# Kernel optimization log

Hardware: AMD Instinct MI355X
Metric: run time of the kernel (lower is better)

## Reference

```python
import jax, jax.numpy as jnp
import numpy as np

B, T, D, H = 4096, 100, 64, 128
N_RK4 = 4  # fixed RK4 substeps per observation gap (deterministic stand-in for adaptive odeint)


def setup_inputs() -> dict:
    key = jax.random.key(0)
    ks = jax.random.split(key, 12)
    x_seq = jax.random.normal(ks[0], (B, T, D), dtype=jnp.float32)
    # strictly increasing shared timestamps (source only uses t_seq[0, :])
    t0 = jnp.cumsum(jax.random.uniform(ks[1], (T,), dtype=jnp.float32) * 0.1 + 0.01)
    t_seq = jnp.broadcast_to(t0, (B, T))
    s_h = 1.0 / np.sqrt(H)
    s_d = 1.0 / np.sqrt(D)
    # ODE func: f(h) = tanh(h W1^T + b1) W2^T + b2
    W1 = jax.random.normal(ks[2], (H, H), jnp.float32) * s_h
    b1 = jnp.zeros((H,), jnp.float32)
    W2 = jax.random.normal(ks[3], (H, H), jnp.float32) * s_h * 0.1
    b2 = jnp.zeros((H,), jnp.float32)
    # GRUCell params (PyTorch layout: [3H, in])
    W_ih = jax.random.normal(ks[4], (3 * H, D), jnp.float32) * s_d
    W_hh = jax.random.normal(ks[5], (3 * H, H), jnp.float32) * s_h
    b_ih = jax.random.normal(ks[6], (3 * H,), jnp.float32) * s_h
    b_hh = jax.random.normal(ks[7], (3 * H,), jnp.float32) * s_h
    W_mu = jax.random.normal(ks[8], (H, H), jnp.float32) * s_h
    b_mu = jnp.zeros((H,), jnp.float32)
    W_lv = jax.random.normal(ks[9], (H, H), jnp.float32) * s_h
    b_lv = jnp.zeros((H,), jnp.float32)
    return dict(x_seq=x_seq, t_seq=t_seq, W1=W1, b1=b1, W2=W2, b2=b2,
                W_ih=W_ih, W_hh=W_hh, b_ih=b_ih, b_hh=b_hh,
                W_mu=W_mu, b_mu=b_mu, W_lv=W_lv, b_lv=b_lv)


def _odernn(x_seq, t_seq, W1, b1, W2, b2, W_ih, W_hh, b_ih, b_hh, W_mu, b_mu, W_lv, b_lv):
    Hdim = W1.shape[0]

    def f(h):  # ode_func, autonomous
        return jnp.tanh(h @ W1.T + b1) @ W2.T + b2

    def rk4_jump(h, dt):  # integrate dh/dt = f(h) over dt with N_RK4 substeps
        sub = dt / N_RK4  # scalar
        for _ in range(N_RK4):
            k1 = f(h)
            k2 = f(h + 0.5 * sub * k1)
            k3 = f(h + 0.5 * sub * k2)
            k4 = f(h + sub * k3)
            h = h + (sub / 6.0) * (k1 + 2.0 * k2 + 2.0 * k3 + k4)
        return h

    def gru(x, h):
        gi = x @ W_ih.T + b_ih  # [B, 3H]
        gh = h @ W_hh.T + b_hh
        i_r, i_z, i_n = jnp.split(gi, 3, axis=-1)
        h_r, h_z, h_n = jnp.split(gh, 3, axis=-1)
        r = jax.nn.sigmoid(i_r + h_r)
        z = jax.nn.sigmoid(i_z + h_z)
        n = jnp.tanh(i_n + r * h_n)
        return (1.0 - z) * n + z * h

    t0 = t_seq[0]  # [T] shared times, as in source (t_seq[0, i])
    dt = jnp.concatenate([jnp.zeros((1,), t0.dtype), t0[1:] - t0[:-1]])  # dt[0]=0 -> no jump at i=0
    h0 = jnp.zeros((x_seq.shape[0], Hdim), x_seq.dtype)

    def step(h, inp):
        x_i, dt_i = inp
        h = rk4_jump(h, dt_i)
        h = gru(x_i, h)
        return h, None

    h, _ = jax.lax.scan(step, h0, (jnp.swapaxes(x_seq, 0, 1), dt))
    mu = h @ W_mu.T + b_mu
    logvar = h @ W_lv.T + b_lv
    return mu, logvar


def reference(x_seq, t_seq, W1, b1, W2, b2, W_ih, W_hh, b_ih, b_hh, W_mu, b_mu, W_lv, b_lv):
    return _odernn(x_seq, t_seq, W1, b1, W2, b2, W_ih, W_hh, b_ih, b_hh, W_mu, b_mu, W_lv, b_lv)
```

## Files before the change

kernel.cpp:

```cpp
#include <hip/hip_runtime.h>

#define Bn 4096
#define Tn 100
#define Dn 64
#define Hn 128

typedef _Float16 half8v __attribute__((ext_vector_type(8)));
typedef _Float16 half4v __attribute__((ext_vector_type(4)));
typedef float    float4v __attribute__((ext_vector_type(4)));
typedef float    float2v __attribute__((ext_vector_type(2)));

__device__ __forceinline__ float fast_tanh(float x) {
    float e = __expf(x + x);
    return 1.0f - 2.0f * __builtin_amdgcn_rcpf(e + 1.0f);
}
__device__ __forceinline__ float fast_sig(float x) {
    return __builtin_amdgcn_rcpf(1.0f + __expf(-x));
}
__device__ __forceinline__ float4v tanh4(float4v u) {
    float4v a;
#pragma unroll
    for (int r = 0; r < 4; r++) a[r] = fast_tanh(u[r]);
    return a;
}
__device__ __forceinline__ half4v pack4(float4v v) {
    half4v p;
#pragma unroll
    for (int r = 0; r < 4; r++) p[r] = (_Float16)v[r];
    return p;
}

__device__ __forceinline__ half8v load_wfrag(const float* __restrict__ W, int ld, int n, int k) {
    const float* p = W + (size_t)n * ld + k;
    float4v a = *(const float4v*)p;
    float4v b = *(const float4v*)(p + 4);
    half8v r;
    r[0] = (_Float16)a[0]; r[1] = (_Float16)a[1]; r[2] = (_Float16)a[2]; r[3] = (_Float16)a[3];
    r[4] = (_Float16)b[0]; r[5] = (_Float16)b[1]; r[6] = (_Float16)b[2]; r[7] = (_Float16)b[3];
    return r;
}

__global__ __launch_bounds__(512) void odernn_kernel(
    const float* __restrict__ x_seq, const float* __restrict__ t_seq,
    const float* __restrict__ W1,   const float* __restrict__ b1,
    const float* __restrict__ W2,   const float* __restrict__ b2,
    const float* __restrict__ W_ih, const float* __restrict__ W_hh,
    const float* __restrict__ b_ih, const float* __restrict__ b_hh,
    const float* __restrict__ W_mu, const float* __restrict__ b_mu,
    const float* __restrict__ W_lv, const float* __restrict__ b_lv,
    float* __restrict__ out)
{
    __shared__ _Float16 vbuf[16 * 136];
    __shared__ _Float16 abuf[2][16 * 136];
    __shared__ _Float16 xbuf[16 * 72];
    __shared__ float    ts_l[Tn];
    __shared__ float    c1s[Hn];

    const int tid  = threadIdx.x;
    const int lane = tid & 63;
    const int w    = tid >> 6;
    const int q    = lane >> 4;
    const int m    = lane & 15;
    const int blk  = blockIdx.x;

    if (tid < Tn) ts_l[tid] = t_seq[tid];
    for (int i = tid; i < 16 * 136; i += 512) vbuf[i] = (_Float16)0.f;
    if (tid < Hn) {
        float acc = 0.f;
        const float* r1 = W1 + (size_t)tid * Hn;
#pragma unroll 4
        for (int j = 0; j < Hn; j++) acc += b2[j] * r1[j];
        c1s[tid] = acc;
    }

    const int n0 = 16 * w + m;
    half8v w1f[4], w2f[4], whhf[3][4], wihf[3][2];
#pragma unroll
    for (int kt = 0; kt < 4; kt++) {
        w1f[kt] = load_wfrag(W1, Hn, n0, 32 * kt + q * 8);
        w2f[kt] = load_wfrag(W2, Hn, n0, 32 * kt + q * 8);
    }
#pragma unroll
    for (int g = 0; g < 3; g++) {
        int n = 128 * g + n0;
#pragma unroll
        for (int kt = 0; kt < 4; kt++) whhf[g][kt] = load_wfrag(W_hh, Hn, n, 32 * kt + q * 8);
#pragma unroll
        for (int kt = 0; kt < 2; kt++) wihf[g][kt] = load_wfrag(W_ih, Dn, n, 32 * kt + q * 8);
    }
    float4v b1q = *(const float4v*)(b1 + 16 * w + q * 4);
    float4v b2q = *(const float4v*)(b2 + 16 * w + q * 4);
    float4v bihq[3], bhhq[3];
#pragma unroll
    for (int g = 0; g < 3; g++) {
        bihq[g] = *(const float4v*)(b_ih + 128 * g + 16 * w + q * 4);
        bhhq[g] = *(const float4v*)(b_hh + 128 * g + 16 * w + q * 4);
    }

    float4v accM[4][2];
#pragma unroll
    for (int kt = 0; kt < 4; kt++) {
        float4v zz = {0.f, 0.f, 0.f, 0.f};
        accM[kt][0] = zz; accM[kt][1] = zz;
    }
    {
        const float* w1row = W1 + (size_t)n0 * Hn;
        for (int j = 0; j < Hn; j++) {
            float w1v = w1row[j];
            const float* w2r = W2 + (size_t)j * Hn + q * 8;
#pragma unroll
            for (int kt = 0; kt < 4; kt++) {
                float4v aa = *(const float4v*)(w2r + 32 * kt);
                float4v bb = *(const float4v*)(w2r + 32 * kt + 4);
#pragma unroll
                for (int r = 0; r < 4; r++) {
                    accM[kt][0][r] += w1v * aa[r];
                    accM[kt][1][r] += w1v * bb[r];
                }
            }
        }
    }
    half8v w21f[4];
#pragma unroll
    for (int kt = 0; kt < 4; kt++) {
#pragma unroll
        for (int r = 0; r < 4; r++) {
            w21f[kt][r]     = (_Float16)accM[kt][0][r];
            w21f[kt][r + 4] = (_Float16)accM[kt][1][r];
        }
    }

    float4v h = {0.f, 0.f, 0.f, 0.f};

    const int xrow = tid >> 5;
    const int xcol = (tid & 31) * 2;
    const float* xptr = x_seq + (size_t)(blk * 16 + xrow) * (Tn * Dn) + xcol;
    float2v xreg = *(const float2v*)xptr;

    const int wslot = m * 136 + 16 * w + q * 4;

    auto gemm4 = [&](const half8v* Wf, const _Float16* base, float4v cin) -> float4v {
        const _Float16* p = base + m * 136 + q * 8;
        half8v bf0 = *(const half8v*)(p);
        half8v bf1 = *(const half8v*)(p + 32);
        half8v bf2 = *(const half8v*)(p + 64);
        half8v bf3 = *(const half8v*)(p + 96);
        float4v o1 = cin;
        float4v o2 = {0.f, 0.f, 0.f, 0.f};
        o1 = __builtin_amdgcn_mfma_f32_16x16x32_f16(Wf[0], bf0, o1, 0, 0, 0);
        o2 = __builtin_amdgcn_mfma_f32_16x16x32_f16(Wf[2], bf2, o2, 0, 0, 0);
        o1 = __builtin_amdgcn_mfma_f32_16x16x32_f16(Wf[1], bf1, o1, 0, 0, 0);
        o2 = __builtin_amdgcn_mfma_f32_16x16x32_f16(Wf[3], bf3, o2, 0, 0, 0);
#pragma unroll
        for (int r = 0; r < 4; r++) o1[r] += o2[r];
        return o1;
    };

    float4v c1q;
    __syncthreads();
#pragma unroll
    for (int r = 0; r < 4; r++) c1q[r] = c1s[16 * w + q * 4 + r];
    const float4v zero4 = {0.f, 0.f, 0.f, 0.f};

#pragma unroll 1
    for (int t = 0; t < Tn; ++t) {
        {
            _Float16* xp = xbuf + xrow * 72 + xcol;
            xp[0] = (_Float16)xreg[0]; xp[1] = (_Float16)xreg[1];
        }
        float tc  = ts_l[t];
        float tp  = (t > 0) ? ts_l[t - 1] : tc;
        float sub = (tc - tp) * 0.25f;
        float hs  = 0.5f * sub;
        float s6  = sub * (1.0f / 6.0f);
        __syncthreads();
        if (t + 1 < Tn) xreg = *(const float2v*)(xptr + (t + 1) * Dn);

        float4v gi[3];
        {
            const _Float16* xp = xbuf + m * 72 + q * 8;
            half8v xf0 = *(const half8v*)(xp);
            half8v xf1 = *(const half8v*)(xp + 32);
#pragma unroll
            for (int g = 0; g < 3; g++) {
                float4v acc = bihq[g];
                acc = __builtin_amdgcn_mfma_f32_16x16x32_f16(wihf[g][0], xf0, acc, 0, 0, 0);
                acc = __builtin_amdgcn_mfma_f32_16x16x32_f16(wihf[g][1], xf1, acc, 0, 0, 0);
                gi[g] = acc;
            }
        }
        float4v u_h = gemm4(w1f, vbuf, b1q);

        if (sub != 0.0f) {
            float4v Abar = zero4;
#pragma unroll 1
            for (int s = 0; s < 4; s++) {
                float4v a1 = tanh4(u_h);
                float4v A  = a1;
                *(half4v*)(abuf[0] + wslot) = pack4(a1);
                __syncthreads();
                float4v g = gemm4(w21f, abuf[0], c1q);
                float4v u;
#pragma unroll
                for (int r = 0; r < 4; r++) u[r] = u_h[r] + hs * g[r];
                float4v a2 = tanh4(u);
#pragma unroll
                for (int r = 0; r < 4; r++) A[r] += 2.0f * a2[r];
                *(half4v*)(abuf[1] + wslot) = pack4(a2);
                __syncthreads();
                g = gemm4(w21f, abuf[1], c1q);
#pragma unroll
                for (int r = 0; r < 4; r++) u[r] = u_h[r] + hs * g[r];
                float4v a3 = tanh4(u);
#pragma unroll
                for (int r = 0; r < 4; r++) A[r] += 2.0f * a3[r];
                *(half4v*)(abuf[0] + wslot) = pack4(a3);
                __syncthreads();
                g = gemm4(w21f, abuf[0], c1q);
#pragma unroll
                for (int r = 0; r < 4; r++) u[r] = u_h[r] + sub * g[r];
                float4v a4 = tanh4(u);
#pragma unroll
                for (int r = 0; r < 4; r++) A[r] += a4[r];
                *(half4v*)(abuf[1] + wslot) = pack4(A);
                __syncthreads();
                g = gemm4(w21f, abuf[1], zero4);
#pragma unroll
                for (int r = 0; r < 4; r++) {
                    u_h[r]  += s6 * g[r] + sub * c1q[r];
                    Abar[r] += A[r];
                }
            }
            *(half4v*)(abuf[0] + wslot) = pack4(Abar);
            __syncthreads();
            float4v gw = gemm4(w2f, abuf[0], zero4);
            float fourSub = 4.0f * sub;
#pragma unroll
            for (int r = 0; r < 4; r++) h[r] += s6 * gw[r] + fourSub * b2q[r];
            *(half4v*)(vbuf + wslot) = pack4(h);
            __syncthreads();
        }

        float4v gh[3];
        {
            const _Float16* p = vbuf + m * 136 + q * 8;
            half8v bf0 = *(const half8v*)(p);
            half8v bf1 = *(const half8v*)(p + 32);
            half8v bf2 = *(const half8v*)(p + 64);
            half8v bf3 = *(const half8v*)(p + 96);
#pragma unroll
            for (int g = 0; g < 3; g++) {
                float4v acc = bhhq[g];
                acc = __builtin_amdgcn_mfma_f32_16x16x32_f16(whhf[g][0], bf0, acc, 0, 0, 0);
                acc = __builtin_amdgcn_mfma_f32_16x16x32_f16(whhf[g][1], bf1, acc, 0, 0, 0);
                acc = __builtin_amdgcn_mfma_f32_16x16x32_f16(whhf[g][2], bf2, acc, 0, 0, 0);
                acc = __builtin_amdgcn_mfma_f32_16x16x32_f16(whhf[g][3], bf3, acc, 0, 0, 0);
                gh[g] = acc;
            }
        }
        __syncthreads();

        {
            half4v pk;
#pragma unroll
            for (int r = 0; r < 4; r++) {
                float rr = fast_sig(gi[0][r] + gh[0][r]);
                float zz = fast_sig(gi[1][r] + gh[1][r]);
                float nn = fast_tanh(gi[2][r] + rr * gh[2][r]);
                float hv = (1.0f - zz) * nn + zz * h[r];
                h[r] = hv;
                pk[r] = (_Float16)hv;
            }
            *(half4v*)(vbuf + wslot) = pk;
        }
    }

    __syncthreads();

#pragma unroll
    for (int mat = 0; mat < 2; mat++) {
        const float* Wm = mat ? W_lv : W_mu;
        const float* bm = mat ? b_lv : b_mu;
        float4v acc = *(const float4v*)(bm + 16 * w + q * 4);
        const _Float16* p = vbuf + m * 136 + q * 8;
#pragma unroll
        for (int kt = 0; kt < 4; kt++) {
            half8v af = load_wfrag(Wm, Hn, n0, 32 * kt + q * 8);
            acc = __builtin_amdgcn_mfma_f32_16x16x32_f16(af, *(const half8v*)(p + kt * 32), acc, 0, 0, 0);
        }
        *(float4v*)(out + (size_t)mat * Bn * Hn + (size_t)(blk * 16 + m) * Hn + 16 * w + q * 4) = acc;
    }
}

extern "C" void kernel_launch(void* const* d_in, const int* in_sizes, int n_in,
                              void* d_out, int out_size, void* d_ws, size_t ws_size,
                              hipStream_t stream) {
    (void)in_sizes; (void)n_in; (void)d_ws; (void)ws_size; (void)out_size;
    odernn_kernel<<<dim3(Bn / 16), dim3(512), 0, stream>>>(
        (const float*)d_in[0],  (const float*)d_in[1],  (const float*)d_in[2],
        (const float*)d_in[3],  (const float*)d_in[4],  (const float*)d_in[5],
        (const float*)d_in[6],  (const float*)d_in[7],  (const float*)d_in[8],
        (const float*)d_in[9],  (const float*)d_in[10], (const float*)d_in[11],
        (const float*)d_in[12], (const float*)d_in[13], (float*)d_out);
}
```

Measured before the change: 811.2 us.

## Fold W_hh into ODE jump, use FP8 MFMA for inner ODE GEMMs

Precomputes W_hh·W2 and W_hh·b2 so the GRU hidden-gate projection is computed from the pre-jump state plus a correction from the averaged tanh activations. This removes the separate h write and barrier after the RK4 jump and lets the W1 and W_hh GEMMs on the old state run together. The RK4 inner GEMMs and the correction GEMMs switch from fp16 to fp8 MFMA with a fixed scale of 64 and a permuted shared-memory layout. Launch bounds now request two blocks per CU. The risk is accuracy loss from fp8 weights and activations, plus register pressure from the extra fragments.

```diff
diff --git a/kernel.cpp b/kernel.cpp
--- a/kernel.cpp
+++ b/kernel.cpp
@@ -9,6 +9,7 @@
 typedef _Float16 half4v __attribute__((ext_vector_type(4)));
 typedef float    float4v __attribute__((ext_vector_type(4)));
 typedef float    float2v __attribute__((ext_vector_type(2)));
+typedef long     long2v  __attribute__((ext_vector_type(2)));
 
 __device__ __forceinline__ float fast_tanh(float x) {
     float e = __expf(x + x);
@@ -28,6 +29,16 @@
 #pragma unroll
     for (int r = 0; r < 4; r++) p[r] = (_Float16)v[r];
     return p;
+}
+__device__ __forceinline__ int pack_fp8x4(float a, float b, float c, float d) {
+    int v = __builtin_amdgcn_cvt_pk_fp8_f32(a, b, 0, false);
+    v = __builtin_amdgcn_cvt_pk_fp8_f32(c, d, v, true);
+    return v;
+}
+__device__ __forceinline__ long pack_fp8x8s(float4v a, float4v b, float s) {
+    int lo = pack_fp8x4(a[0]*s, a[1]*s, a[2]*s, a[3]*s);
+    int hi = pack_fp8x4(b[0]*s, b[1]*s, b[2]*s, b[3]*s);
+    return (long)(((unsigned long long)(unsigned)hi << 32) | (unsigned)lo);
 }
 
 __device__ __forceinline__ half8v load_wfrag(const float* __restrict__ W, int ld, int n, int k) {
@@ -40,7 +51,7 @@
     return r;
 }
 
-__global__ __launch_bounds__(512) void odernn_kernel(
+__global__ __launch_bounds__(512, 2) void odernn_kernel(
     const float* __restrict__ x_seq, const float* __restrict__ t_seq,
     const float* __restrict__ W1,   const float* __restrict__ b1,
     const float* __restrict__ W2,   const float* __restrict__ b2,
@@ -51,10 +62,11 @@
     float* __restrict__ out)
 {
     __shared__ _Float16 vbuf[16 * 136];
-    __shared__ _Float16 abuf[2][16 * 136];
+    __shared__ __attribute__((aligned(16))) unsigned char abuf8[2][16 * 144];
     __shared__ _Float16 xbuf[16 * 72];
     __shared__ float    ts_l[Tn];
     __shared__ float    c1s[Hn];
+    __shared__ float    c2s[3 * Hn];
 
     const int tid  = threadIdx.x;
     const int lane = tid & 63;
@@ -71,15 +83,19 @@
 #pragma unroll 4
         for (int j = 0; j < Hn; j++) acc += b2[j] * r1[j];
         c1s[tid] = acc;
+    } else {
+        int i = tid - Hn;
+        float acc = 0.f;
+        const float* rh = W_hh + (size_t)i * Hn;
+#pragma unroll 4
+        for (int j = 0; j < Hn; j++) acc += rh[j] * b2[j];
+        c2s[i] = acc;
     }
 
     const int n0 = 16 * w + m;
-    half8v w1f[4], w2f[4], whhf[3][4], wihf[3][2];
-#pragma unroll
-    for (int kt = 0; kt < 4; kt++) {
-        w1f[kt] = load_wfrag(W1, Hn, n0, 32 * kt + q * 8);
-        w2f[kt] = load_wfrag(W2, Hn, n0, 32 * kt + q * 8);
-    }
+    half8v w1f[4], whhf[3][4], wihf[3][2];
+#pragma unroll
+    for (int kt = 0; kt < 4; kt++) w1f[kt] = load_wfrag(W1, Hn, n0, 32 * kt + q * 8);
 #pragma unroll
     for (int g = 0; g < 3; g++) {
         int n = 128 * g + n0;
@@ -97,37 +113,41 @@
         bhhq[g] = *(const float4v*)(b_hh + 128 * g + 16 * w + q * 4);
     }
 
-    float4v accM[4][2];
+    float4v aM[4][2], aG[3][4][2];
 #pragma unroll
     for (int kt = 0; kt < 4; kt++) {
         float4v zz = {0.f, 0.f, 0.f, 0.f};
-        accM[kt][0] = zz; accM[kt][1] = zz;
+        aM[kt][0] = zz; aM[kt][1] = zz;
+#pragma unroll
+        for (int g = 0; g < 3; g++) { aG[g][kt][0] = zz; aG[g][kt][1] = zz; }
     }
     {
-        const float* w1row = W1 + (size_t)n0 * Hn;
+        const float* w1row = W1   + (size_t)n0 * Hn;
+        const float* h0row = W_hh + (size_t)n0 * Hn;
+        const float* h1row = W_hh + (size_t)(128 + n0) * Hn;
+        const float* h2row = W_hh + (size_t)(256 + n0) * Hn;
         for (int j = 0; j < Hn; j++) {
-            float w1v = w1row[j];
+            float s0 = w1row[j], s1 = h0row[j], s2 = h1row[j], s3 = h2row[j];
             const float* w2r = W2 + (size_t)j * Hn + q * 8;
 #pragma unroll
             for (int kt = 0; kt < 4; kt++) {
                 float4v aa = *(const float4v*)(w2r + 32 * kt);
                 float4v bb = *(const float4v*)(w2r + 32 * kt + 4);
-#pragma unroll
-                for (int r = 0; r < 4; r++) {
-                    accM[kt][0][r] += w1v * aa[r];
-                    accM[kt][1][r] += w1v * bb[r];
-                }
-            }
-        }
-    }
-    half8v w21f[4];
+                aM[kt][0] += s0 * aa;      aM[kt][1] += s0 * bb;
+                aG[0][kt][0] += s1 * aa;   aG[0][kt][1] += s1 * bb;
+                aG[1][kt][0] += s2 * aa;   aG[1][kt][1] += s2 * bb;
+                aG[2][kt][0] += s3 * aa;   aG[2][kt][1] += s3 * bb;
+            }
+        }
+    }
+    long w21f8[4], m2f8[3][4], w2f8[4];
 #pragma unroll
     for (int kt = 0; kt < 4; kt++) {
-#pragma unroll
-        for (int r = 0; r < 4; r++) {
-            w21f[kt][r]     = (_Float16)accM[kt][0][r];
-            w21f[kt][r + 4] = (_Float16)accM[kt][1][r];
-        }
+        w21f8[kt] = pack_fp8x8s(aM[kt][0], aM[kt][1], 64.0f);
+#pragma unroll
+        for (int g = 0; g < 3; g++) m2f8[g][kt] = pack_fp8x8s(aG[g][kt][0], aG[g][kt][1], 64.0f);
+        const float* p = W2 + (size_t)n0 * Hn + 32 * kt + q * 8;
+        w2f8[kt] = pack_fp8x8s(*(const float4v*)p, *(const float4v*)(p + 4), 64.0f);
     }
 
     float4v h = {0.f, 0.f, 0.f, 0.f};
@@ -138,29 +158,33 @@
     float2v xreg = *(const float2v*)xptr;
 
     const int wslot = m * 136 + 16 * w + q * 4;
-
-    auto gemm4 = [&](const half8v* Wf, const _Float16* base, float4v cin) -> float4v {
-        const _Float16* p = base + m * 136 + q * 8;
-        half8v bf0 = *(const half8v*)(p);
-        half8v bf1 = *(const half8v*)(p + 32);
-        half8v bf2 = *(const half8v*)(p + 64);
-        half8v bf3 = *(const half8v*)(p + 96);
-        float4v o1 = cin;
-        float4v o2 = {0.f, 0.f, 0.f, 0.f};
-        o1 = __builtin_amdgcn_mfma_f32_16x16x32_f16(Wf[0], bf0, o1, 0, 0, 0);
-        o2 = __builtin_amdgcn_mfma_f32_16x16x32_f16(Wf[2], bf2, o2, 0, 0, 0);
-        o1 = __builtin_amdgcn_mfma_f32_16x16x32_f16(Wf[1], bf1, o1, 0, 0, 0);
-        o2 = __builtin_amdgcn_mfma_f32_16x16x32_f16(Wf[3], bf3, o2, 0, 0, 0);
-#pragma unroll
-        for (int r = 0; r < 4; r++) o1[r] += o2[r];
-        return o1;
+    const int ppos = 64 * (w >> 2) + 16 * ((2 * (w & 3) + (q >> 1)) & 3)
+                   + 8 * ((w >> 1) & 1) + 4 * (q & 1);
+    const float4v zero4 = {0.f, 0.f, 0.f, 0.f};
+
+    auto store_a = [&](int pp, float4v v) {
+        *(int*)(abuf8[pp] + m * 144 + ppos) = pack_fp8x4(v[0], v[1], v[2], v[3]);
     };
-
-    float4v c1q;
+    auto gemm8 = [&](const long* Wf, int pp) -> float4v {
+        const unsigned char* p = abuf8[pp] + m * 144;
+        long2v L0 = *(const long2v*)(p + q * 16);
+        long2v L1 = *(const long2v*)(p + 64 + q * 16);
+        float4v o1 = zero4, o2 = zero4;
+        o1 = __builtin_amdgcn_mfma_f32_16x16x32_fp8_fp8(Wf[0], L0[0], o1, 0, 0, 0);
+        o2 = __builtin_amdgcn_mfma_f32_16x16x32_fp8_fp8(Wf[2], L1[0], o2, 0, 0, 0);
+        o1 = __builtin_amdgcn_mfma_f32_16x16x32_fp8_fp8(Wf[1], L0[1], o1, 0, 0, 0);
+        o2 = __builtin_amdgcn_mfma_f32_16x16x32_fp8_fp8(Wf[3], L1[1], o2, 0, 0, 0);
+        return o1 + o2;
+    };
+
+    float4v c1q, c2q[3];
     __syncthreads();
 #pragma unroll
     for (int r = 0; r < 4; r++) c1q[r] = c1s[16 * w + q * 4 + r];
-    const float4v zero4 = {0.f, 0.f, 0.f, 0.f};
+#pragma unroll
+    for (int g = 0; g < 3; g++)
+#pragma unroll
+        for (int r = 0; r < 4; r++) c2q[g][r] = c2s[128 * g + 16 * w + q * 4 + r];
 
 #pragma unroll 1
     for (int t = 0; t < Tn; ++t) {
@@ -168,15 +192,18 @@
             _Float16* xp = xbuf + xrow * 72 + xcol;
             xp[0] = (_Float16)xreg[0]; xp[1] = (_Float16)xreg[1];
         }
-        float tc  = ts_l[t];
-        float tp  = (t > 0) ? ts_l[t - 1] : tc;
-        float sub = (tc - tp) * 0.25f;
-        float hs  = 0.5f * sub;
-        float s6  = sub * (1.0f / 6.0f);
+        float tc   = ts_l[t];
+        float tp   = (t > 0) ? ts_l[t - 1] : tc;
+        float sub  = (tc - tp) * 0.25f;
+        float hs   = 0.5f * sub;
+        float s6   = sub * (1.0f / 6.0f);
+        float hs64 = hs * (1.0f / 64.0f);
+        float sb64 = sub * (1.0f / 64.0f);
+        float s664 = s6 * (1.0f / 64.0f);
         __syncthreads();
         if (t + 1 < Tn) xreg = *(const float2v*)(xptr + (t + 1) * Dn);
 
-        float4v gi[3];
+        float4v gi[3], gh[3], u_h;
         {
             const _Float16* xp = xbuf + m * 72 + q * 8;
             half8v xf0 = *(const half8v*)(xp);
@@ -188,66 +215,17 @@
                 acc = __builtin_amdgcn_mfma_f32_16x16x32_f16(wihf[g][1], xf1, acc, 0, 0, 0);
                 gi[g] = acc;
             }
-        }
-        float4v u_h = gemm4(w1f, vbuf, b1q);
-
-        if (sub != 0.0f) {
-            float4v Abar = zero4;
-#pragma unroll 1
-            for (int s = 0; s < 4; s++) {
-                float4v a1 = tanh4(u_h);
-                float4v A  = a1;
-                *(half4v*)(abuf[0] + wslot) = pack4(a1);
-                __syncthreads();
-                float4v g = gemm4(w21f, abuf[0], c1q);
-                float4v u;
-#pragma unroll
-                for (int r = 0; r < 4; r++) u[r] = u_h[r] + hs * g[r];
-                float4v a2 = tanh4(u);
-#pragma unroll
-                for (int r = 0; r < 4; r++) A[r] += 2.0f * a2[r];
-                *(half4v*)(abuf[1] + wslot) = pack4(a2);
-                __syncthreads();
-                g = gemm4(w21f, abuf[1], c1q);
-#pragma unroll
-                for (int r = 0; r < 4; r++) u[r] = u_h[r] + hs * g[r];
-                float4v a3 = tanh4(u);
-#pragma unroll
-                for (int r = 0; r < 4; r++) A[r] += 2.0f * a3[r];
-                *(half4v*)(abuf[0] + wslot) = pack4(a3);
-                __syncthreads();
-                g = gemm4(w21f, abuf[0], c1q);
-#pragma unroll
-                for (int r = 0; r < 4; r++) u[r] = u_h[r] + sub * g[r];
-                float4v a4 = tanh4(u);
-#pragma unroll
-                for (int r = 0; r < 4; r++) A[r] += a4[r];
-                *(half4v*)(abuf[1] + wslot) = pack4(A);
-                __syncthreads();
-                g = gemm4(w21f, abuf[1], zero4);
-#pragma unroll
-                for (int r = 0; r < 4; r++) {
-                    u_h[r]  += s6 * g[r] + sub * c1q[r];
-                    Abar[r] += A[r];
-                }
-            }
-            *(half4v*)(abuf[0] + wslot) = pack4(Abar);
-            __syncthreads();
-            float4v gw = gemm4(w2f, abuf[0], zero4);
-            float fourSub = 4.0f * sub;
-#pragma unroll
-            for (int r = 0; r < 4; r++) h[r] += s6 * gw[r] + fourSub * b2q[r];
-            *(half4v*)(vbuf + wslot) = pack4(h);
-            __syncthreads();
-        }
-
-        float4v gh[3];
-        {
-            const _Float16* p = vbuf + m * 136 + q * 8;
-            half8v bf0 = *(const half8v*)(p);
-            half8v bf1 = *(const half8v*)(p + 32);
-            half8v bf2 = *(const half8v*)(p + 64);
-            half8v bf3 = *(const half8v*)(p + 96);
+            const _Float16* vp = vbuf + m * 136 + q * 8;
+            half8v bf0 = *(const half8v*)(vp);
+            half8v bf1 = *(const half8v*)(vp + 32);
+            half8v bf2 = *(const half8v*)(vp + 64);
+            half8v bf3 = *(const half8v*)(vp + 96);
+            float4v o1 = b1q, o2 = zero4;
+            o1 = __builtin_amdgcn_mfma_f32_16x16x32_f16(w1f[0], bf0, o1, 0, 0, 0);
+            o2 = __builtin_amdgcn_mfma_f32_16x16x32_f16(w1f[2], bf2, o2, 0, 0, 0);
+            o1 = __builtin_amdgcn_mfma_f32_16x16x32_f16(w1f[1], bf1, o1, 0, 0, 0);
+            o2 = __builtin_amdgcn_mfma_f32_16x16x32_f16(w1f[3], bf3, o2, 0, 0, 0);
+            u_h = o1 + o2;
 #pragma unroll
             for (int g = 0; g < 3; g++) {
                 float4v acc = bhhq[g];
@@ -258,7 +236,62 @@
                 gh[g] = acc;
             }
         }
-        __syncthreads();
+
+        if (sub != 0.0f) {
+            float4v Abar = zero4;
+#pragma unroll 1
+            for (int s = 0; s < 4; s++) {
+                float4v a1 = tanh4(u_h);
+                float4v A = a1;
+                store_a(0, a1);
+                __syncthreads();
+                float4v g = gemm8(w21f8, 0);
+                float4v u = u_h + hs64 * g + hs * c1q;
+                float4v a2 = tanh4(u);
+                A += 2.0f * a2;
+                store_a(1, a2);
+                __syncthreads();
+                g = gemm8(w21f8, 1);
+                u = u_h + hs64 * g + hs * c1q;
+                float4v a3 = tanh4(u);
+                A += 2.0f * a3;
+                store_a(0, a3);
+                __syncthreads();
+                g = gemm8(w21f8, 0);
+                u = u_h + sb64 * g + sub * c1q;
+                float4v a4 = tanh4(u);
+                A += a4;
+                store_a(1, A);
+                __syncthreads();
+                g = gemm8(w21f8, 1);
+                u_h += s664 * g + sub * c1q;
+                Abar += A;
+            }
+            store_a(0, Abar);
+            __syncthreads();
+            {
+                const unsigned char* p = abuf8[0] + m * 144;
+                long2v L0 = *(const long2v*)(p + q * 16);
+                long2v L1 = *(const long2v*)(p + 64 + q * 16);
+                float4v o1 = zero4, o2 = zero4;
+                o1 = __builtin_amdgcn_mfma_f32_16x16x32_fp8_fp8(w2f8[0], L0[0], o1, 0, 0, 0);
+                o2 = __builtin_amdgcn_mfma_f32_16x16x32_fp8_fp8(w2f8[2], L1[0], o2, 0, 0, 0);
+                o1 = __builtin_amdgcn_mfma_f32_16x16x32_fp8_fp8(w2f8[1], L0[1], o1, 0, 0, 0);
+                o2 = __builtin_amdgcn_mfma_f32_16x16x32_fp8_fp8(w2f8[3], L1[1], o2, 0, 0, 0);
+                float4v hd = o1 + o2;
+                float fs = 4.0f * sub;
+                h += s664 * hd + fs * b2q;
+#pragma unroll
+                for (int g = 0; g < 3; g++) {
+                    float4v p1 = zero4, p2 = zero4;
+                    p1 = __builtin_amdgcn_mfma_f32_16x16x32_fp8_fp8(m2f8[g][0], L0[0], p1, 0, 0, 0);
+                    p2 = __builtin_amdgcn_mfma_f32_16x16x32_fp8_fp8(m2f8[g][2], L1[0], p2, 0, 0, 0);
+                    p1 = __builtin_amdgcn_mfma_f32_16x16x32_fp8_fp8(m2f8[g][1], L0[1], p1, 0, 0, 0);
+                    p2 = __builtin_amdgcn_mfma_f32_16x16x32_fp8_fp8(m2f8[g][3], L1[1], p2, 0, 0, 0);
+                    gh[g] += s664 * (p1 + p2) + fs * c2q[g];
+                }
+            }
+        }
 
         {
             half4v pk;
```

Measured after the change: 1.048 ms. +29.2%, slower.

## Skip final RK4 state update, move W_ih fragments to LDS, force two waves per EU

Applied to the files above, without the earlier changes.

The last RK4 substep's u_h update (one GEMM and one barrier) is skipped because its result is never used. Only Abar feeds the W2 projection of h. The W_ih weight fragments move from registers to shared memory and are reloaded each timestep, which frees VGPRs. A waves_per_eu(2,2) attribute is added so the compiler targets two waves per EU. The trade is extra LDS reads per step and a possible register-allocation change.

```diff
diff --git a/kernel.cpp b/kernel.cpp
--- a/kernel.cpp
+++ b/kernel.cpp
@@ -5,8 +5,8 @@
 #define Dn 64
 #define Hn 128
 
-typedef _Float16 half8v __attribute__((ext_vector_type(8)));
-typedef _Float16 half4v __attribute__((ext_vector_type(4)));
+typedef _Float16 half8v  __attribute__((ext_vector_type(8)));
+typedef _Float16 half4v  __attribute__((ext_vector_type(4)));
 typedef float    float4v __attribute__((ext_vector_type(4)));
 typedef float    float2v __attribute__((ext_vector_type(2)));
 
@@ -40,7 +40,8 @@
     return r;
 }
 
-__global__ __launch_bounds__(512) void odernn_kernel(
+__global__ __attribute__((amdgpu_flat_work_group_size(512, 512), amdgpu_waves_per_eu(2, 2)))
+void odernn_kernel(
     const float* __restrict__ x_seq, const float* __restrict__ t_seq,
     const float* __restrict__ W1,   const float* __restrict__ b1,
     const float* __restrict__ W2,   const float* __restrict__ b2,
@@ -50,10 +51,11 @@
     const float* __restrict__ W_lv, const float* __restrict__ b_lv,
     float* __restrict__ out)
 {
+    __shared__ float    ts_l[Tn];
     __shared__ _Float16 vbuf[16 * 136];
     __shared__ _Float16 abuf[2][16 * 136];
     __shared__ _Float16 xbuf[16 * 72];
-    __shared__ float    ts_l[Tn];
+    __shared__ _Float16 wih_l[8 * 6 * 64 * 8];
     __shared__ float    c1s[Hn];
 
     const int tid  = threadIdx.x;
@@ -72,22 +74,26 @@
         for (int j = 0; j < Hn; j++) acc += b2[j] * r1[j];
         c1s[tid] = acc;
     }
+#pragma unroll
+    for (int f = 0; f < 6; f++) {
+        int g = f >> 1, kt = f & 1;
+        half8v fr = load_wfrag(W_ih, Dn, 128 * g + 16 * w + m, 32 * kt + q * 8);
+        *(half8v*)(wih_l + ((w * 6 + f) * 64 + lane) * 8) = fr;
+    }
 
     const int n0 = 16 * w + m;
-    half8v w1f[4], w2f[4], whhf[3][4], wihf[3][2];
+    half8v w1f[4], w2f[4], whhf[3][4];
 #pragma unroll
     for (int kt = 0; kt < 4; kt++) {
         w1f[kt] = load_wfrag(W1, Hn, n0, 32 * kt + q * 8);
         w2f[kt] = load_wfrag(W2, Hn, n0, 32 * kt + q * 8);
     }
 #pragma unroll
-    for (int g = 0; g < 3; g++) {
-        int n = 128 * g + n0;
-#pragma unroll
-        for (int kt = 0; kt < 4; kt++) whhf[g][kt] = load_wfrag(W_hh, Hn, n, 32 * kt + q * 8);
-#pragma unroll
-        for (int kt = 0; kt < 2; kt++) wihf[g][kt] = load_wfrag(W_ih, Dn, n, 32 * kt + q * 8);
-    }
+    for (int g = 0; g < 3; g++)
+#pragma unroll
+        for (int kt = 0; kt < 4; kt++)
+            whhf[g][kt] = load_wfrag(W_hh, Hn, 128 * g + n0, 32 * kt + q * 8);
+
     float4v b1q = *(const float4v*)(b1 + 16 * w + q * 4);
     float4v b2q = *(const float4v*)(b2 + 16 * w + q * 4);
     float4v bihq[3], bhhq[3];
@@ -97,11 +103,11 @@
         bhhq[g] = *(const float4v*)(b_hh + 128 * g + 16 * w + q * 4);
     }
 
-    float4v accM[4][2];
+    float4v aM[4][2];
 #pragma unroll
     for (int kt = 0; kt < 4; kt++) {
         float4v zz = {0.f, 0.f, 0.f, 0.f};
-        accM[kt][0] = zz; accM[kt][1] = zz;
+        aM[kt][0] = zz; aM[kt][1] = zz;
     }
     {
         const float* w1row = W1 + (size_t)n0 * Hn;
@@ -110,13 +116,8 @@
             const float* w2r = W2 + (size_t)j * Hn + q * 8;
 #pragma unroll
             for (int kt = 0; kt < 4; kt++) {
-                float4v aa = *(const float4v*)(w2r + 32 * kt);
-                float4v bb = *(const float4v*)(w2r + 32 * kt + 4);
-#pragma unroll
-                for (int r = 0; r < 4; r++) {
-                    accM[kt][0][r] += w1v * aa[r];
-                    accM[kt][1][r] += w1v * bb[r];
-                }
+                aM[kt][0] += w1v * *(const float4v*)(w2r + 32 * kt);
+                aM[kt][1] += w1v * *(const float4v*)(w2r + 32 * kt + 4);
             }
         }
     }
@@ -125,12 +126,13 @@
     for (int kt = 0; kt < 4; kt++) {
 #pragma unroll
         for (int r = 0; r < 4; r++) {
-            w21f[kt][r]     = (_Float16)accM[kt][0][r];
-            w21f[kt][r + 4] = (_Float16)accM[kt][1][r];
+            w21f[kt][r]     = (_Float16)aM[kt][0][r];
+            w21f[kt][r + 4] = (_Float16)aM[kt][1][r];
         }
     }
 
     float4v h = {0.f, 0.f, 0.f, 0.f};
+    const float4v zero4 = {0.f, 0.f, 0.f, 0.f};
 
     const int xrow = tid >> 5;
     const int xcol = (tid & 31) * 2;
@@ -146,21 +148,18 @@
         half8v bf2 = *(const half8v*)(p + 64);
         half8v bf3 = *(const half8v*)(p + 96);
         float4v o1 = cin;
-        float4v o2 = {0.f, 0.f, 0.f, 0.f};
+        float4v o2 = zero4;
         o1 = __builtin_amdgcn_mfma_f32_16x16x32_f16(Wf[0], bf0, o1, 0, 0, 0);
         o2 = __builtin_amdgcn_mfma_f32_16x16x32_f16(Wf[2], bf2, o2, 0, 0, 0);
         o1 = __builtin_amdgcn_mfma_f32_16x16x32_f16(Wf[1], bf1, o1, 0, 0, 0);
         o2 = __builtin_amdgcn_mfma_f32_16x16x32_f16(Wf[3], bf3, o2, 0, 0, 0);
-#pragma unroll
-        for (int r = 0; r < 4; r++) o1[r] += o2[r];
-        return o1;
+        return o1 + o2;
     };
 
     float4v c1q;
     __syncthreads();
 #pragma unroll
     for (int r = 0; r < 4; r++) c1q[r] = c1s[16 * w + q * 4 + r];
-    const float4v zero4 = {0.f, 0.f, 0.f, 0.f};
 
 #pragma unroll 1
     for (int t = 0; t < Tn; ++t) {
@@ -184,8 +183,10 @@
 #pragma unroll
             for (int g = 0; g < 3; g++) {
                 float4v acc = bihq[g];
-                acc = __builtin_amdgcn_mfma_f32_16x16x32_f16(wihf[g][0], xf0, acc, 0, 0, 0);
-                acc = __builtin_amdgcn_mfma_f32_16x16x32_f16(wihf[g][1], xf1, acc, 0, 0, 0);
+                half8v wf0 = *(const half8v*)(wih_l + ((w * 6 + g * 2 + 0) * 64 + lane) * 8);
+                half8v wf1 = *(const half8v*)(wih_l + ((w * 6 + g * 2 + 1) * 64 + lane) * 8);
+                acc = __builtin_amdgcn_mfma_f32_16x16x32_f16(wf0, xf0, acc, 0, 0, 0);
+                acc = __builtin_amdgcn_mfma_f32_16x16x32_f16(wf1, xf1, acc, 0, 0, 0);
                 gi[g] = acc;
             }
         }
@@ -196,58 +197,48 @@
 #pragma unroll 1
             for (int s = 0; s < 4; s++) {
                 float4v a1 = tanh4(u_h);
-                float4v A  = a1;
+                float4v A = a1;
                 *(half4v*)(abuf[0] + wslot) = pack4(a1);
                 __syncthreads();
-                float4v g = gemm4(w21f, abuf[0], c1q);
-                float4v u;
-#pragma unroll
-                for (int r = 0; r < 4; r++) u[r] = u_h[r] + hs * g[r];
+                float4v g = gemm4(w21f, abuf[0], zero4);
+                float4v u = u_h + hs * g + hs * c1q;
                 float4v a2 = tanh4(u);
-#pragma unroll
-                for (int r = 0; r < 4; r++) A[r] += 2.0f * a2[r];
+                A += 2.0f * a2;
                 *(half4v*)(abuf[1] + wslot) = pack4(a2);
                 __syncthreads();
-                g = gemm4(w21f, abuf[1], c1q);
-#pragma unroll
-                for (int r = 0; r < 4; r++) u[r] = u_h[r] + hs * g[r];
+                g = gemm4(w21f, abuf[1], zero4);
+                u = u_h + hs * g + hs * c1q;
                 float4v a3 = tanh4(u);
-#pragma unroll
-                for (int r = 0; r < 4; r++) A[r] += 2.0f * a3[r];
+                A += 2.0f * a3;
                 *(half4v*)(abuf[0] + wslot) = pack4(a3);
                 __syncthreads();
-                g = gemm4(w21f, abuf[0], c1q);
-#pragma unroll
-                for (int r = 0; r < 4; r++) u[r] = u_h[r] + sub * g[r];
+                g = gemm4(w21f, abuf[0], zero4);
+                u = u_h + sub * g + sub * c1q;
                 float4v a4 = tanh4(u);
-#pragma unroll
-                for (int r = 0; r < 4; r++) A[r] += a4[r];
-                *(half4v*)(abuf[1] + wslot) = pack4(A);
-                __syncthreads();
-                g = gemm4(w21f, abuf[1], zero4);
-#pragma unroll
-                for (int r = 0; r < 4; r++) {
-                    u_h[r]  += s6 * g[r] + sub * c1q[r];
-                    Abar[r] += A[r];
+                A += a4;
+                Abar += A;
+                if (s < 3) {
+                    *(half4v*)(abuf[1] + wslot) = pack4(A);
+                    __syncthreads();
+                    g = gemm4(w21f, abuf[1], zero4);
+                    u_h += s6 * g + sub * c1q;
                 }
             }
-            *(half4v*)(abuf[0] + wslot) = pack4(Abar);
+            *(half4v*)(abuf[1] + wslot) = pack4(Abar);
             __syncthreads();
-            float4v gw = gemm4(w2f, abuf[0], zero4);
-            float fourSub = 4.0f * sub;
-#pragma unroll
-            for (int r = 0; r < 4; r++) h[r] += s6 * gw[r] + fourSub * b2q[r];
+            float4v gw = gemm4(w2f, abuf[1], zero4);
+            h += s6 * gw + (4.0f * sub) * b2q;
             *(half4v*)(vbuf + wslot) = pack4(h);
             __syncthreads();
         }
 
         float4v gh[3];
         {
-            const _Float16* p = vbuf + m * 136 + q * 8;
-            half8v bf0 = *(const half8v*)(p);
-            half8v bf1 = *(const half8v*)(p + 32);
-            half8v bf2 = *(const half8v*)(p + 64);
-            half8v bf3 = *(const half8v*)(p + 96);
+            const _Float16* vp = vbuf + m * 136 + q * 8;
+            half8v bf0 = *(const half8v*)(vp);
+            half8v bf1 = *(const half8v*)(vp + 32);
+            half8v bf2 = *(const half8v*)(vp + 64);
+            half8v bf3 = *(const half8v*)(vp + 96);
 #pragma unroll
             for (int g = 0; g < 3; g++) {
                 float4v acc = bhhq[g];
```

Result: no change. 819.0 us (+1.0%).
